# Kernel optimization log

Measured on AMD Instinct MI355X. Metric: run time of the kernel, lower is better.

Reference implementation:

```python
import jax, jax.numpy as jnp
import numpy as np

B = 131072
HIDDEN = 20
N_HID_LAYERS = 8  # 1 input layer (3->20) + 7 hidden (20->20), then head 20->2
G_GRAV = 9.81


def _xavier(key, fan_in, fan_out, shape):
    lim = float(np.sqrt(6.0 / (fan_in + fan_out)))
    return jax.random.uniform(key, shape, jnp.float32, -lim, lim)


def setup_inputs() -> dict:
    key = jax.random.key(0)
    ks = jax.random.split(key, 9)
    return {
        "x": jax.random.normal(ks[0], (B,), jnp.float32),
        "y": jax.random.normal(ks[1], (B,), jnp.float32),
        "t": jax.random.normal(ks[2], (B,), jnp.float32),
        "u": jax.random.normal(ks[3], (B,), jnp.float32),
        "v": jax.random.normal(ks[4], (B,), jnp.float32),
        "W_in": _xavier(ks[5], 3, HIDDEN, (3, HIDDEN)),
        "b_in": jnp.zeros((HIDDEN,), jnp.float32),
        "W_h": _xavier(ks[6], HIDDEN, HIDDEN, (N_HID_LAYERS - 1, HIDDEN, HIDDEN)),
        "b_h": jnp.zeros((N_HID_LAYERS - 1, HIDDEN), jnp.float32),
        "W_out": _xavier(ks[7], HIDDEN, 2, (HIDDEN, 2)),
        "b_out": jnp.zeros((2,), jnp.float32),
        "lambda1": jnp.zeros((), jnp.float32),
        "lambda2": jnp.zeros((), jnp.float32),
    }


def _pinn(x, y, t, u, v, W_in, b_in, W_h, b_h, W_out, b_out, lambda1, lambda2):
    def net(z):  # z: (3,) -> (2,) = (psi, p)
        h = jnp.tanh(z @ W_in + b_in)
        for i in range(W_h.shape[0]):
            h = jnp.tanh(h @ W_h[i] + b_h[i])
        return h @ W_out + b_out

    psi_fn = lambda z: net(z)[0]
    p_fn = lambda z: net(z)[1]

    def per_point(z):
        G = jax.grad(psi_fn)(z)                       # (3,)  dpsi/dz
        H = jax.jacfwd(jax.grad(psi_fn))(z)           # (3,3) d2psi
        T = jax.jacfwd(jax.jacfwd(jax.grad(psi_fn)))(z)  # (3,3,3) d3psi
        return G, H, T, p_fn(z), jax.grad(p_fn)(z)

    z = jnp.stack([x, y, t], axis=1)  # (B,3), axes: 0=x, 1=y, 2=t
    G, H, T, p_pred, Gp = jax.vmap(per_point)(z)

    u_pred = G[:, 1]          # dpsi/dy
    v_pred = -G[:, 0]         # -dpsi/dx
    u_x, u_y, u_t = H[:, 1, 0], H[:, 1, 1], H[:, 1, 2]
    v_x, v_y, v_t = -H[:, 0, 0], -H[:, 0, 1], -H[:, 0, 2]
    u_xx, u_yy = T[:, 1, 0, 0], T[:, 1, 1, 1]
    v_xx, v_yy = -T[:, 0, 0, 0], -T[:, 0, 1, 1]
    p_x, p_y = Gp[:, 0], Gp[:, 1]

    f_u = lambda1 * (u_t + u_pred * u_x + v_pred * u_y) + p_x - lambda2 * (u_xx + u_yy)
    f_v = (lambda1 * (v_t + u_pred * v_x + v_pred * v_y) - lambda1 * G_GRAV
           + p_y - lambda2 * (v_xx + v_yy))

    preds = jnp.stack([p_pred, u_pred, v_pred], axis=1)  # (B,3)
    loss = (jnp.sum((u - u_pred) ** 2) + jnp.sum((v - v_pred) ** 2)
            + jnp.sum(f_u ** 2) + jnp.sum(f_v ** 2))
    return preds, loss


def reference(x, y, t, u, v, W_in, b_in, W_h, b_h, W_out, b_out, lambda1, lambda2):
    return _pinn(x, y, t, u, v, W_in, b_in, W_h, b_h, W_out, b_out, lambda1, lambda2)
```

## Files before the change

kernel.cpp:

```cpp
#include <hip/hip_runtime.h>

typedef float v2f __attribute__((ext_vector_type(2)));

constexpr int BN   = 131072;
constexpr int HID  = 20;
constexpr int NLAY = 7;

constexpr int OFF_WH   = 0;
constexpr int OFF_BH   = 2800;
constexpr int OFF_WIN  = 2940;
constexpr int OFF_BIN  = 3000;
constexpr int OFF_WOUT = 3020;
constexpr int OFF_BOUT = 3060;
constexpr int LDS_TOT  = 3064;

enum { S_PX = 0, S_PXX, S_PXXX, S_P, S_GPX,
       S_PY, S_PYY, S_PYYY, S_GPY,
       S_D2P, S_D3P, S_D3M, S_XT, S_YT, NSLOT };

__device__ __forceinline__ float fast_tanh(float a) {
    float e = __builtin_amdgcn_exp2f(a * 2.8853900817779268f);
    float r = __builtin_amdgcn_rcpf(e + 1.0f);
    return __builtin_fmaf(-2.0f, r, 1.0f);
}
__device__ __forceinline__ v2f tanh2(v2f a) {
    v2f r; r.x = fast_tanh(a.x); r.y = fast_tanh(a.y); return r;
}
__device__ __forceinline__ v2f splat(float s) { v2f r = {s, s}; return r; }
#define FMA2(a, b, c) __builtin_elementwise_fma((a), (b), (c))

__device__ __forceinline__ void pk_fma_lo(v2f& acc, const v2f s, const v2f w) {
    asm("v_pk_fma_f32 %0, %1, %2, %0 op_sel:[0,0,0] op_sel_hi:[0,1,1]"
        : "+v"(acc) : "v"(s), "v"(w));
}
__device__ __forceinline__ void pk_fma_hi(v2f& acc, const v2f s, const v2f w) {
    asm("v_pk_fma_f32 %0, %1, %2, %0 op_sel:[1,0,0] op_sel_hi:[1,1,1]"
        : "+v"(acc) : "v"(s), "v"(w));
}

__device__ __forceinline__ void stage_weights(
    float* smem, const float* Win, const float* bin, const float* Wh,
    const float* bh, const float* Wout, const float* bout)
{
    const int tid = threadIdx.x;
    for (int i = tid; i < 2800; i += 256) smem[OFF_WH + i] = Wh[i];
    for (int i = tid; i < 140;  i += 256) smem[OFF_BH + i] = bh[i];
    if (tid < 60) smem[OFF_WIN  + tid] = Win[tid];
    if (tid < 20) smem[OFF_BIN  + tid] = bin[tid];
    if (tid < 40) smem[OFF_WOUT + tid] = Wout[tid];
    if (tid < 2)  smem[OFF_BOUT + tid] = bout[tid];
    __syncthreads();
}

template<bool BIASED>
__device__ __forceinline__ void sweep2(const v2f (&S1)[10], const v2f (&S2)[10],
                                       v2f (&A1)[10], v2f (&A2)[10],
                                       const float* __restrict__ Wl,
                                       const float* __restrict__ bl)
{
    #pragma unroll
    for (int j = 0; j < 10; ++j) {
        if (BIASED) { A1[j].x = bl[2*j]; A1[j].y = bl[2*j+1]; }
        else        A1[j] = splat(0.f);
        A2[j] = splat(0.f);
    }
    #pragma unroll
    for (int i = 0; i < 10; ++i) {
        const float* r0 = &Wl[(2 * i) * HID];
        const float* r1 = &Wl[(2 * i + 1) * HID];
        #pragma unroll
        for (int ob = 0; ob < 5; ++ob) {
            float4 w0 = *(const float4*)&r0[4 * ob];
            float4 w1 = *(const float4*)&r1[4 * ob];
            v2f w0a = {w0.x, w0.y}, w0b = {w0.z, w0.w};
            v2f w1a = {w1.x, w1.y}, w1b = {w1.z, w1.w};
            pk_fma_lo(A1[2*ob],   S1[i], w0a);
            pk_fma_lo(A1[2*ob+1], S1[i], w0b);
            pk_fma_hi(A1[2*ob],   S1[i], w1a);
            pk_fma_hi(A1[2*ob+1], S1[i], w1b);
            pk_fma_lo(A2[2*ob],   S2[i], w0a);
            pk_fma_lo(A2[2*ob+1], S2[i], w0b);
            pk_fma_hi(A2[2*ob],   S2[i], w1a);
            pk_fma_hi(A2[2*ob+1], S2[i], w1b);
        }
    }
}

__device__ __forceinline__ void sweep3(const v2f (&S1)[10], const v2f (&S2)[10],
                                       const v2f (&S3)[10],
                                       v2f (&A1)[10], v2f (&A2)[10], v2f (&A3)[10],
                                       const float* __restrict__ Wl,
                                       const float* __restrict__ bl)
{
    #pragma unroll
    for (int j = 0; j < 10; ++j) {
        A1[j].x = bl[2*j]; A1[j].y = bl[2*j+1];
        A2[j] = splat(0.f);
        A3[j] = splat(0.f);
    }
    #pragma unroll
    for (int i = 0; i < 10; ++i) {
        const float* r0 = &Wl[(2 * i) * HID];
        const float* r1 = &Wl[(2 * i + 1) * HID];
        #pragma unroll
        for (int ob = 0; ob < 5; ++ob) {
            float4 w0 = *(const float4*)&r0[4 * ob];
            float4 w1 = *(const float4*)&r1[4 * ob];
            v2f w0a = {w0.x, w0.y}, w0b = {w0.z, w0.w};
            v2f w1a = {w1.x, w1.y}, w1b = {w1.z, w1.w};
            pk_fma_lo(A1[2*ob],   S1[i], w0a);
            pk_fma_lo(A1[2*ob+1], S1[i], w0b);
            pk_fma_hi(A1[2*ob],   S1[i], w1a);
            pk_fma_hi(A1[2*ob+1], S1[i], w1b);
            pk_fma_lo(A2[2*ob],   S2[i], w0a);
            pk_fma_lo(A2[2*ob+1], S2[i], w0b);
            pk_fma_hi(A2[2*ob],   S2[i], w1a);
            pk_fma_hi(A2[2*ob+1], S2[i], w1b);
            pk_fma_lo(A3[2*ob],   S3[i], w0a);
            pk_fma_lo(A3[2*ob+1], S3[i], w0b);
            pk_fma_hi(A3[2*ob],   S3[i], w1a);
            pk_fma_hi(A3[2*ob+1], S3[i], w1b);
        }
    }
}

__global__ __launch_bounds__(256, 2) void pinn_fast(
    const float* __restrict__ x, const float* __restrict__ y, const float* __restrict__ t,
    const float* __restrict__ u, const float* __restrict__ v,
    const float* __restrict__ Win, const float* __restrict__ bin,
    const float* __restrict__ Wh,  const float* __restrict__ bh,
    const float* __restrict__ Wout,const float* __restrict__ bout,
    const float* __restrict__ lam1p, const float* __restrict__ lam2p,
    float* __restrict__ out)
{
    if (lam1p[0] != 0.0f || lam2p[0] != 0.0f) return;

    __shared__ __align__(16) float smem[LDS_TOT];
    __shared__ float wsum[4];
    stage_weights(smem, Win, bin, Wh, bh, Wout, bout);

    const int tid = threadIdx.x;
    const int pt  = blockIdx.x * 256 + tid;
    const float xv = x[pt], yv = y[pt], tv = t[pt];
    const v2f xv2 = splat(xv), yv2 = splat(yv), tv2 = splat(tv);

    v2f V[10], DX[10], DY[10];

    #pragma unroll
    for (int j = 0; j < 10; ++j) {
        v2f w0 = *(const v2f*)&smem[OFF_WIN + 2*j];
        v2f w1 = *(const v2f*)&smem[OFF_WIN + HID + 2*j];
        v2f w2 = *(const v2f*)&smem[OFF_WIN + 2*HID + 2*j];
        v2f av = *(const v2f*)&smem[OFF_BIN + 2*j];
        av = FMA2(xv2, w0, av);
        av = FMA2(yv2, w1, av);
        av = FMA2(tv2, w2, av);
        v2f s  = tanh2(av);
        v2f s1 = 1.0f - s * s;
        V[j]  = s;
        DX[j] = s1 * w0;
        DY[j] = s1 * w1;
    }

    #pragma unroll 1
    for (int l = 0; l < NLAY; ++l) {
        const float* Wl = &smem[OFF_WH + l * (HID * HID)];
        const float* bl = &smem[OFF_BH + l * HID];
        v2f aV[10], aX[10], aY[10];
        sweep3(V, DX, DY, aV, aX, aY, Wl, bl);
        #pragma unroll
        for (int j = 0; j < 10; ++j) {
            v2f s  = tanh2(aV[j]);
            v2f s1 = 1.0f - s * s;
            V[j]  = s;
            DX[j] = s1 * aX[j];
            DY[j] = s1 * aY[j];
        }
    }

    v2f dX = splat(0.f), dY = splat(0.f), dP = splat(0.f),
        dPX = splat(0.f), dPY = splat(0.f);
    #pragma unroll
    for (int j = 0; j < 10; ++j) {
        v2f w0j = {smem[OFF_WOUT + 4*j],     smem[OFF_WOUT + 4*j + 2]};
        v2f w1j = {smem[OFF_WOUT + 4*j + 1], smem[OFF_WOUT + 4*j + 3]};
        dX  = FMA2(DX[j], w0j, dX);
        dY  = FMA2(DY[j], w0j, dY);
        dP  = FMA2(V[j],  w1j, dP);
        dPX = FMA2(DX[j], w1j, dPX);
        dPY = FMA2(DY[j], w1j, dPY);
    }
    const float psi_x = dX.x + dX.y;
    const float psi_y = dY.x + dY.y;
    const float pv    = smem[OFF_BOUT + 1] + dP.x + dP.y;
    const float p_x   = dPX.x + dPX.y;
    const float p_y   = dPY.x + dPY.y;

    const float u_pred = psi_y;
    const float v_pred = -psi_x;
    const float f_u = p_x;
    const float f_v = p_y;

    out[3*pt+0] = pv;
    out[3*pt+1] = u_pred;
    out[3*pt+2] = v_pred;

    const float du = u[pt] - u_pred;
    const float dv = v[pt] - v_pred;
    float term = du * du + dv * dv + f_u * f_u + f_v * f_v;

    #pragma unroll
    for (int off = 32; off > 0; off >>= 1) term += __shfl_down(term, off);
    const int lane = tid & 63, wid = tid >> 6;
    if (lane == 0) wsum[wid] = term;
    __syncthreads();
    if (tid == 0) atomicAdd(&out[3*BN], wsum[0] + wsum[1] + wsum[2] + wsum[3]);
}

__global__ __launch_bounds__(256, 3) void pinn_jets6(
    const float* __restrict__ x, const float* __restrict__ y, const float* __restrict__ t,
    const float* __restrict__ Win, const float* __restrict__ bin,
    const float* __restrict__ Wh,  const float* __restrict__ bh,
    const float* __restrict__ Wout,const float* __restrict__ bout,
    const float* __restrict__ lam1p, const float* __restrict__ lam2p,
    float* __restrict__ ws)
{
    if (lam1p[0] == 0.0f && lam2p[0] == 0.0f) return;

    __shared__ __align__(16) float smem[LDS_TOT];
    stage_weights(smem, Win, bin, Wh, bh, Wout, bout);

    const int pt    = blockIdx.x * 256 + threadIdx.x;
    const int slice = blockIdx.y;

    const float xv = x[pt], yv = y[pt], tv = t[pt];
    const v2f xv2 = splat(xv), yv2 = splat(yv), tv2 = splat(tv);

    if (slice < 4) {
        const float DXT[4] = {1.f, 0.f, 1.f,  1.f};
        const float DYT[4] = {0.f, 1.f, 1.f, -1.f};
        const v2f dxv = splat(DXT[slice]), dyv = splat(DYT[slice]);

        v2f V[10], D1[10], D2[10], D3[10];

        #pragma unroll
        for (int j = 0; j < 10; ++j) {
            v2f w0 = *(const v2f*)&smem[OFF_WIN + 2*j];
            v2f w1 = *(const v2f*)&smem[OFF_WIN + HID + 2*j];
            v2f w2 = *(const v2f*)&smem[OFF_WIN + 2*HID + 2*j];
            v2f av = *(const v2f*)&smem[OFF_BIN + 2*j];
            av = FMA2(xv2, w0, av);
            av = FMA2(yv2, w1, av);
            av = FMA2(tv2, w2, av);
            v2f a1 = dxv * w0;
            a1 = FMA2(dyv, w1, a1);
            v2f s  = tanh2(av);
            v2f s2 = s * s;
            v2f s1 = 1.0f - s2;
            v2f f2 = -2.0f * s * s1;
            v2f f3 = s1 * (4.0f * s2 - 2.0f * s1);
            v2f a1sq = a1 * a1;
            V[j]  = s;
            D1[j] = s1 * a1;
            D2[j] = f2 * a1sq;
            D3[j] = f3 * a1sq * a1;
        }

        #pragma unroll 1
        for (int l = 0; l < NLAY; ++l) {
            const float* Wl = &smem[OFF_WH + l * (HID * HID)];
            const float* bl = &smem[OFF_BH + l * HID];
            v2f aV[10], a1[10];
            sweep2<true >(V,  D1, aV, a1, Wl, bl);
            v2f a2[10], a3[10];
            sweep2<false>(D2, D3, a2, a3, Wl, bl);
            #pragma unroll
            for (int j = 0; j < 10; ++j) {
                v2f s  = tanh2(aV[j]);
                v2f s2 = s * s;
                v2f s1 = 1.0f - s2;
                v2f f2 = -2.0f * s * s1;
                v2f f3 = s1 * (4.0f * s2 - 2.0f * s1);
                v2f u1 = a1[j];
                v2f u1sq = u1 * u1;
                V[j]  = s;
                D1[j] = s1 * u1;
                D2[j] = s1 * a2[j] + f2 * u1sq;
                D3[j] = s1 * a3[j] + 3.0f * f2 * (u1 * a2[j]) + f3 * u1sq * u1;
            }
        }

        v2f d1 = splat(0.f), d2 = splat(0.f), d3 = splat(0.f),
            dP = splat(0.f), dP1 = splat(0.f);
        #pragma unroll
        for (int j = 0; j < 10; ++j) {
            v2f w0j = {smem[OFF_WOUT + 4*j],     smem[OFF_WOUT + 4*j + 2]};
            v2f w1j = {smem[OFF_WOUT + 4*j + 1], smem[OFF_WOUT + 4*j + 3]};
            d1  = FMA2(D1[j], w0j, d1);
            d2  = FMA2(D2[j], w0j, d2);
            d3  = FMA2(D3[j], w0j, d3);
            dP  = FMA2(V[j],  w1j, dP);
            dP1 = FMA2(D1[j], w1j, dP1);
        }
        const float r1 = d1.x + d1.y;
        const float r2 = d2.x + d2.y;
        const float r3 = d3.x + d3.y;

        switch (slice) {
            case 0:
                ws[S_PX  *BN+pt] = r1;
                ws[S_PXX *BN+pt] = r2;
                ws[S_PXXX*BN+pt] = r3;
                ws[S_P   *BN+pt] = smem[OFF_BOUT + 1] + dP.x + dP.y;
                ws[S_GPX *BN+pt] = dP1.x + dP1.y;
                break;
            case 1:
                ws[S_PY  *BN+pt] = r1;
                ws[S_PYY *BN+pt] = r2;
                ws[S_PYYY*BN+pt] = r3;
                ws[S_GPY *BN+pt] = dP1.x + dP1.y;
                break;
            case 2:
                ws[S_D2P *BN+pt] = r2;
                ws[S_D3P *BN+pt] = r3;
                break;
            default:
                ws[S_D3M *BN+pt] = r3;
                break;
        }
    } else {
        v2f V[10], DA[10], DT[10], DAT[10];

        #pragma unroll
        for (int j = 0; j < 10; ++j) {
            v2f w0 = *(const v2f*)&smem[OFF_WIN + 2*j];
            v2f w1 = *(const v2f*)&smem[OFF_WIN + HID + 2*j];
            v2f w2 = *(const v2f*)&smem[OFF_WIN + 2*HID + 2*j];
            v2f av = *(const v2f*)&smem[OFF_BIN + 2*j];
            av = FMA2(xv2, w0, av);
            av = FMA2(yv2, w1, av);
            av = FMA2(tv2, w2, av);
            v2f wa = (slice == 4) ? w0 : w1;
            v2f s  = tanh2(av);
            v2f s1 = 1.0f - s * s;
            v2f f2 = -2.0f * s * s1;
            V[j]   = s;
            DA[j]  = s1 * wa;
            DT[j]  = s1 * w2;
            DAT[j] = f2 * wa * w2;
        }

        #pragma unroll 1
        for (int l = 0; l < NLAY; ++l) {
            const float* Wl = &smem[OFF_WH + l * (HID * HID)];
            const float* bl = &smem[OFF_BH + l * HID];
            v2f aV[10], aA[10];
            sweep2<true >(V,  DA,  aV, aA, Wl, bl);
            v2f aT[10], aAT[10];
            sweep2<false>(DT, DAT, aT, aAT, Wl, bl);
            #pragma unroll
            for (int j = 0; j < 10; ++j) {
                v2f s  = tanh2(aV[j]);
                v2f s1 = 1.0f - s * s;
                v2f f2 = -2.0f * s * s1;
                V[j]   = s;
                DA[j]  = s1 * aA[j];
                DT[j]  = s1 * aT[j];
                DAT[j] = f2 * (aA[j] * aT[j]) + s1 * aAT[j];
            }
        }

        v2f dAT = splat(0.f);
        #pragma unroll
        for (int j = 0; j < 10; ++j) {
            v2f w0j = {smem[OFF_WOUT + 4*j], smem[OFF_WOUT + 4*j + 2]};
            dAT = FMA2(DAT[j], w0j, dAT);
        }
        const float r = dAT.x + dAT.y;
        if (slice == 4) ws[S_XT*BN+pt] = r;
        else            ws[S_YT*BN+pt] = r;
    }
}

__global__ __launch_bounds__(256) void pinn_combine(
    const float* __restrict__ ws,
    const float* __restrict__ u, const float* __restrict__ v,
    const float* __restrict__ lam1p, const float* __restrict__ lam2p,
    float* __restrict__ out)
{
    if (lam1p[0] == 0.0f && lam2p[0] == 0.0f) return;

    __shared__ float wsum[4];
    const int tid = threadIdx.x;
    const int pt  = blockIdx.x * 256 + tid;

    const float psi_x   = ws[S_PX  *BN+pt];
    const float psi_xx  = ws[S_PXX *BN+pt];
    const float psi_xxx = ws[S_PXXX*BN+pt];
    const float pv      = ws[S_P   *BN+pt];
    const float p_x     = ws[S_GPX *BN+pt];
    const float psi_y   = ws[S_PY  *BN+pt];
    const float psi_yy  = ws[S_PYY *BN+pt];
    const float psi_yyy = ws[S_PYYY*BN+pt];
    const float p_y     = ws[S_GPY *BN+pt];
    const float d2p     = ws[S_D2P *BN+pt];
    const float d3p     = ws[S_D3P *BN+pt];
    const float d3m     = ws[S_D3M *BN+pt];
    const float psi_xt  = ws[S_XT  *BN+pt];
    const float psi_yt  = ws[S_YT  *BN+pt];

    const float psi_xy  = 0.5f * (d2p - psi_xx - psi_yy);
    const float psi_xxy = (d3p - d3m - 2.0f * psi_yyy) * (1.0f / 6.0f);
    const float psi_xyy = (d3p + d3m - 2.0f * psi_xxx) * (1.0f / 6.0f);

    const float u_pred = psi_y;
    const float v_pred = -psi_x;
    const float u_x = psi_xy,  u_y = psi_yy,  u_t = psi_yt;
    const float v_x = -psi_xx, v_y = -psi_xy, v_t = -psi_xt;
    const float u_xx = psi_xxy, u_yy = psi_yyy;
    const float v_xx = -psi_xxx, v_yy = -psi_xyy;

    const float lam1 = lam1p[0];
    const float lam2 = lam2p[0];

    const float f_u = lam1 * (u_t + u_pred * u_x + v_pred * u_y) + p_x - lam2 * (u_xx + u_yy);
    const float f_v = lam1 * (v_t + u_pred * v_x + v_pred * v_y) - lam1 * 9.81f + p_y
                      - lam2 * (v_xx + v_yy);

    out[3*pt+0] = pv;
    out[3*pt+1] = u_pred;
    out[3*pt+2] = v_pred;

    const float du = u[pt] - u_pred;
    const float dv = v[pt] - v_pred;
    float term = du * du + dv * dv + f_u * f_u + f_v * f_v;

    #pragma unroll
    for (int off = 32; off > 0; off >>= 1) term += __shfl_down(term, off);
    const int lane = tid & 63, wid = tid >> 6;
    if (lane == 0) wsum[wid] = term;
    __syncthreads();
    if (tid == 0) atomicAdd(&out[3*BN], wsum[0] + wsum[1] + wsum[2] + wsum[3]);
}

extern "C" void kernel_launch(void* const* d_in, const int* in_sizes, int n_in,
                              void* d_out, int out_size, void* d_ws, size_t ws_size,
                              hipStream_t stream) {
    const float* x    = (const float*)d_in[0];
    const float* y    = (const float*)d_in[1];
    const float* t    = (const float*)d_in[2];
    const float* u    = (const float*)d_in[3];
    const float* v    = (const float*)d_in[4];
    const float* Win  = (const float*)d_in[5];
    const float* bin  = (const float*)d_in[6];
    const float* Wh   = (const float*)d_in[7];
    const float* bh   = (const float*)d_in[8];
    const float* Wout = (const float*)d_in[9];
    const float* bout = (const float*)d_in[10];
    const float* lam1 = (const float*)d_in[11];
    const float* lam2 = (const float*)d_in[12];

    float* out = (float*)d_out;
    float* ws  = (float*)d_ws;

    hipMemsetAsync(out + 3 * BN, 0, sizeof(float), stream);

    pinn_fast<<<BN / 256, 256, 0, stream>>>(x, y, t, u, v, Win, bin, Wh, bh,
                                            Wout, bout, lam1, lam2, out);
    pinn_jets6<<<dim3(BN / 256, 6), 256, 0, stream>>>(x, y, t, Win, bin, Wh, bh,
                                                      Wout, bout, lam1, lam2, ws);
    pinn_combine<<<BN / 256, 256, 0, stream>>>(ws, u, v, lam1, lam2, out);
}
```

Baseline: 45.91 us.

## Split each point's hidden-layer matvec across two threads with shuffle reduction

Replaces the single-thread-per-point fast kernel with one where each pair of lanes shares a point. Each lane handles half of the input neurons of every 20x20 layer and keeps only 5 packed activation slots. Partial sums are combined with xor-1 shuffles, after which each lane applies tanh to its own half of the outputs. This halves register pressure and doubles the number of threads, aiming at higher occupancy and latency hiding, at the cost of extra cross-lane shuffles per layer and half-idle lanes in the final store and reduction.

```diff
diff --git a/kernel.cpp b/kernel.cpp
--- a/kernel.cpp
+++ b/kernel.cpp
@@ -27,6 +27,9 @@
     v2f r; r.x = fast_tanh(a.x); r.y = fast_tanh(a.y); return r;
 }
 __device__ __forceinline__ v2f splat(float s) { v2f r = {s, s}; return r; }
+__device__ __forceinline__ v2f shflx1(v2f a) {
+    v2f r; r.x = __shfl_xor(a.x, 1); r.y = __shfl_xor(a.y, 1); return r;
+}
 #define FMA2(a, b, c) __builtin_elementwise_fma((a), (b), (c))
 
 __device__ __forceinline__ void pk_fma_lo(v2f& acc, const v2f s, const v2f w) {
@@ -50,6 +53,139 @@
     if (tid < 40) smem[OFF_WOUT + tid] = Wout[tid];
     if (tid < 2)  smem[OFF_BOUT + tid] = bout[tid];
     __syncthreads();
+}
+
+__global__ __launch_bounds__(256, 4) void pinn_fast2(
+    const float* __restrict__ x, const float* __restrict__ y, const float* __restrict__ t,
+    const float* __restrict__ u, const float* __restrict__ v,
+    const float* __restrict__ Win, const float* __restrict__ bin,
+    const float* __restrict__ Wh,  const float* __restrict__ bh,
+    const float* __restrict__ Wout,const float* __restrict__ bout,
+    const float* __restrict__ lam1p, const float* __restrict__ lam2p,
+    float* __restrict__ out)
+{
+    if (lam1p[0] != 0.0f || lam2p[0] != 0.0f) return;
+
+    __shared__ __align__(16) float smem[LDS_TOT];
+    __shared__ float wsum[4];
+    stage_weights(smem, Win, bin, Wh, bh, Wout, bout);
+
+    const int tid  = threadIdx.x;
+    const int half = tid & 1;
+    const int base = 5 * half;
+    const int pt   = blockIdx.x * 128 + (tid >> 1);
+
+    const float xv = x[pt], yv = y[pt], tv = t[pt];
+    const v2f xv2 = splat(xv), yv2 = splat(yv), tv2 = splat(tv);
+
+    v2f V[5], DX[5], DY[5];
+
+    #pragma unroll
+    for (int j = 0; j < 5; ++j) {
+        const int g = base + j;
+        v2f w0 = *(const v2f*)&smem[OFF_WIN + 2*g];
+        v2f w1 = *(const v2f*)&smem[OFF_WIN + HID + 2*g];
+        v2f w2 = *(const v2f*)&smem[OFF_WIN + 2*HID + 2*g];
+        v2f av = *(const v2f*)&smem[OFF_BIN + 2*g];
+        av = FMA2(xv2, w0, av);
+        av = FMA2(yv2, w1, av);
+        av = FMA2(tv2, w2, av);
+        v2f s  = tanh2(av);
+        v2f s1 = 1.0f - s * s;
+        V[j]  = s;
+        DX[j] = s1 * w0;
+        DY[j] = s1 * w1;
+    }
+
+    #pragma unroll 1
+    for (int l = 0; l < NLAY; ++l) {
+        const float* Wl = &smem[OFF_WH + l * (HID * HID)];
+        v2f aV[10], aX[10], aY[10];
+        #pragma unroll
+        for (int k = 0; k < 10; ++k) { aV[k] = splat(0.f); aX[k] = splat(0.f); aY[k] = splat(0.f); }
+        #pragma unroll
+        for (int i = 0; i < 5; ++i) {
+            const float* r0 = &Wl[(2 * (base + i)) * HID];
+            const float* r1 = &Wl[(2 * (base + i) + 1) * HID];
+            #pragma unroll
+            for (int ob = 0; ob < 5; ++ob) {
+                float4 w0 = *(const float4*)&r0[4 * ob];
+                float4 w1 = *(const float4*)&r1[4 * ob];
+                v2f w0a = {w0.x, w0.y}, w0b = {w0.z, w0.w};
+                v2f w1a = {w1.x, w1.y}, w1b = {w1.z, w1.w};
+                pk_fma_lo(aV[2*ob],   V[i],  w0a);
+                pk_fma_lo(aV[2*ob+1], V[i],  w0b);
+                pk_fma_hi(aV[2*ob],   V[i],  w1a);
+                pk_fma_hi(aV[2*ob+1], V[i],  w1b);
+                pk_fma_lo(aX[2*ob],   DX[i], w0a);
+                pk_fma_lo(aX[2*ob+1], DX[i], w0b);
+                pk_fma_hi(aX[2*ob],   DX[i], w1a);
+                pk_fma_hi(aX[2*ob+1], DX[i], w1b);
+                pk_fma_lo(aY[2*ob],   DY[i], w0a);
+                pk_fma_lo(aY[2*ob+1], DY[i], w0b);
+                pk_fma_hi(aY[2*ob],   DY[i], w1a);
+                pk_fma_hi(aY[2*ob+1], DY[i], w1b);
+            }
+        }
+        #pragma unroll
+        for (int k = 0; k < 10; ++k) {
+            aV[k] += shflx1(aV[k]);
+            aX[k] += shflx1(aX[k]);
+            aY[k] += shflx1(aY[k]);
+        }
+        #pragma unroll
+        for (int j = 0; j < 5; ++j) {
+            v2f a0 = half ? aV[5 + j] : aV[j];
+            v2f ax = half ? aX[5 + j] : aX[j];
+            v2f ay = half ? aY[5 + j] : aY[j];
+            a0 += *(const v2f*)&smem[OFF_BH + l * HID + 2 * (base + j)];
+            v2f s  = tanh2(a0);
+            v2f s1 = 1.0f - s * s;
+            V[j]  = s;
+            DX[j] = s1 * ax;
+            DY[j] = s1 * ay;
+        }
+    }
+
+    v2f dX = splat(0.f), dY = splat(0.f), dP = splat(0.f),
+        dPX = splat(0.f), dPY = splat(0.f);
+    #pragma unroll
+    for (int j = 0; j < 5; ++j) {
+        const int g = base + j;
+        v2f w0j = {smem[OFF_WOUT + 4*g],     smem[OFF_WOUT + 4*g + 2]};
+        v2f w1j = {smem[OFF_WOUT + 4*g + 1], smem[OFF_WOUT + 4*g + 3]};
+        dX  = FMA2(DX[j], w0j, dX);
+        dY  = FMA2(DY[j], w0j, dY);
+        dP  = FMA2(V[j],  w1j, dP);
+        dPX = FMA2(DX[j], w1j, dPX);
+        dPY = FMA2(DY[j], w1j, dPY);
+    }
+    float psi_x = dX.x + dX.y;   psi_x += __shfl_xor(psi_x, 1);
+    float psi_y = dY.x + dY.y;   psi_y += __shfl_xor(psi_y, 1);
+    float pv    = dP.x + dP.y;   pv    += __shfl_xor(pv, 1);
+    float p_x   = dPX.x + dPX.y; p_x   += __shfl_xor(p_x, 1);
+    float p_y   = dPY.x + dPY.y; p_y   += __shfl_xor(p_y, 1);
+    pv += smem[OFF_BOUT + 1];
+
+    const float u_pred = psi_y;
+    const float v_pred = -psi_x;
+
+    float term = 0.0f;
+    if (half == 0) {
+        out[3*pt+0] = pv;
+        out[3*pt+1] = u_pred;
+        out[3*pt+2] = v_pred;
+        const float du = u[pt] - u_pred;
+        const float dv = v[pt] - v_pred;
+        term = du * du + dv * dv + p_x * p_x + p_y * p_y;
+    }
+
+    #pragma unroll
+    for (int off = 32; off > 0; off >>= 1) term += __shfl_down(term, off);
+    const int lane = tid & 63, wid = tid >> 6;
+    if (lane == 0) wsum[wid] = term;
+    __syncthreads();
+    if (tid == 0) atomicAdd(&out[3*BN], wsum[0] + wsum[1] + wsum[2] + wsum[3]);
 }
 
 template<bool BIASED>
@@ -84,137 +220,6 @@
             pk_fma_hi(A2[2*ob+1], S2[i], w1b);
         }
     }
-}
-
-__device__ __forceinline__ void sweep3(const v2f (&S1)[10], const v2f (&S2)[10],
-                                       const v2f (&S3)[10],
-                                       v2f (&A1)[10], v2f (&A2)[10], v2f (&A3)[10],
-                                       const float* __restrict__ Wl,
-                                       const float* __restrict__ bl)
-{
-    #pragma unroll
-    for (int j = 0; j < 10; ++j) {
-        A1[j].x = bl[2*j]; A1[j].y = bl[2*j+1];
-        A2[j] = splat(0.f);
-        A3[j] = splat(0.f);
-    }
-    #pragma unroll
-    for (int i = 0; i < 10; ++i) {
-        const float* r0 = &Wl[(2 * i) * HID];
-        const float* r1 = &Wl[(2 * i + 1) * HID];
-        #pragma unroll
-        for (int ob = 0; ob < 5; ++ob) {
-            float4 w0 = *(const float4*)&r0[4 * ob];
-            float4 w1 = *(const float4*)&r1[4 * ob];
-            v2f w0a = {w0.x, w0.y}, w0b = {w0.z, w0.w};
-            v2f w1a = {w1.x, w1.y}, w1b = {w1.z, w1.w};
-            pk_fma_lo(A1[2*ob],   S1[i], w0a);
-            pk_fma_lo(A1[2*ob+1], S1[i], w0b);
-            pk_fma_hi(A1[2*ob],   S1[i], w1a);
-            pk_fma_hi(A1[2*ob+1], S1[i], w1b);
-            pk_fma_lo(A2[2*ob],   S2[i], w0a);
-            pk_fma_lo(A2[2*ob+1], S2[i], w0b);
-            pk_fma_hi(A2[2*ob],   S2[i], w1a);
-            pk_fma_hi(A2[2*ob+1], S2[i], w1b);
-            pk_fma_lo(A3[2*ob],   S3[i], w0a);
-            pk_fma_lo(A3[2*ob+1], S3[i], w0b);
-            pk_fma_hi(A3[2*ob],   S3[i], w1a);
-            pk_fma_hi(A3[2*ob+1], S3[i], w1b);
-        }
-    }
-}
-
-__global__ __launch_bounds__(256, 2) void pinn_fast(
-    const float* __restrict__ x, const float* __restrict__ y, const float* __restrict__ t,
-    const float* __restrict__ u, const float* __restrict__ v,
-    const float* __restrict__ Win, const float* __restrict__ bin,
-    const float* __restrict__ Wh,  const float* __restrict__ bh,
-    const float* __restrict__ Wout,const float* __restrict__ bout,
-    const float* __restrict__ lam1p, const float* __restrict__ lam2p,
-    float* __restrict__ out)
-{
-    if (lam1p[0] != 0.0f || lam2p[0] != 0.0f) return;
-
-    __shared__ __align__(16) float smem[LDS_TOT];
-    __shared__ float wsum[4];
-    stage_weights(smem, Win, bin, Wh, bh, Wout, bout);
-
-    const int tid = threadIdx.x;
-    const int pt  = blockIdx.x * 256 + tid;
-    const float xv = x[pt], yv = y[pt], tv = t[pt];
-    const v2f xv2 = splat(xv), yv2 = splat(yv), tv2 = splat(tv);
-
-    v2f V[10], DX[10], DY[10];
-
-    #pragma unroll
-    for (int j = 0; j < 10; ++j) {
-        v2f w0 = *(const v2f*)&smem[OFF_WIN + 2*j];
-        v2f w1 = *(const v2f*)&smem[OFF_WIN + HID + 2*j];
-        v2f w2 = *(const v2f*)&smem[OFF_WIN + 2*HID + 2*j];
-        v2f av = *(const v2f*)&smem[OFF_BIN + 2*j];
-        av = FMA2(xv2, w0, av);
-        av = FMA2(yv2, w1, av);
-        av = FMA2(tv2, w2, av);
-        v2f s  = tanh2(av);
-        v2f s1 = 1.0f - s * s;
-        V[j]  = s;
-        DX[j] = s1 * w0;
-        DY[j] = s1 * w1;
-    }
-
-    #pragma unroll 1
-    for (int l = 0; l < NLAY; ++l) {
-        const float* Wl = &smem[OFF_WH + l * (HID * HID)];
-        const float* bl = &smem[OFF_BH + l * HID];
-        v2f aV[10], aX[10], aY[10];
-        sweep3(V, DX, DY, aV, aX, aY, Wl, bl);
-        #pragma unroll
-        for (int j = 0; j < 10; ++j) {
-            v2f s  = tanh2(aV[j]);
-            v2f s1 = 1.0f - s * s;
-            V[j]  = s;
-            DX[j] = s1 * aX[j];
-            DY[j] = s1 * aY[j];
-        }
-    }
-
-    v2f dX = splat(0.f), dY = splat(0.f), dP = splat(0.f),
-        dPX = splat(0.f), dPY = splat(0.f);
-    #pragma unroll
-    for (int j = 0; j < 10; ++j) {
-        v2f w0j = {smem[OFF_WOUT + 4*j],     smem[OFF_WOUT + 4*j + 2]};
-        v2f w1j = {smem[OFF_WOUT + 4*j + 1], smem[OFF_WOUT + 4*j + 3]};
-        dX  = FMA2(DX[j], w0j, dX);
-        dY  = FMA2(DY[j], w0j, dY);
-        dP  = FMA2(V[j],  w1j, dP);
-        dPX = FMA2(DX[j], w1j, dPX);
-        dPY = FMA2(DY[j], w1j, dPY);
-    }
-    const float psi_x = dX.x + dX.y;
-    const float psi_y = dY.x + dY.y;
-    const float pv    = smem[OFF_BOUT + 1] + dP.x + dP.y;
-    const float p_x   = dPX.x + dPX.y;
-    const float p_y   = dPY.x + dPY.y;
-
-    const float u_pred = psi_y;
-    const float v_pred = -psi_x;
-    const float f_u = p_x;
-    const float f_v = p_y;
-
-    out[3*pt+0] = pv;
-    out[3*pt+1] = u_pred;
-    out[3*pt+2] = v_pred;
-
-    const float du = u[pt] - u_pred;
-    const float dv = v[pt] - v_pred;
-    float term = du * du + dv * dv + f_u * f_u + f_v * f_v;
-
-    #pragma unroll
-    for (int off = 32; off > 0; off >>= 1) term += __shfl_down(term, off);
-    const int lane = tid & 63, wid = tid >> 6;
-    if (lane == 0) wsum[wid] = term;
-    __syncthreads();
-    if (tid == 0) atomicAdd(&out[3*BN], wsum[0] + wsum[1] + wsum[2] + wsum[3]);
 }
 
 __global__ __launch_bounds__(256, 3) void pinn_jets6(
@@ -465,8 +470,8 @@
 
     hipMemsetAsync(out + 3 * BN, 0, sizeof(float), stream);
 
-    pinn_fast<<<BN / 256, 256, 0, stream>>>(x, y, t, u, v, Win, bin, Wh, bh,
-                                            Wout, bout, lam1, lam2, out);
+    pinn_fast2<<<BN / 128, 256, 0, stream>>>(x, y, t, u, v, Win, bin, Wh, bh,
+                                             Wout, bout, lam1, lam2, out);
     pinn_jets6<<<dim3(BN / 256, 6), 256, 0, stream>>>(x, y, t, Win, bin, Wh, bh,
                                                       Wout, bout, lam1, lam2, ws);
     pinn_combine<<<BN / 256, 256, 0, stream>>>(ws, u, v, lam1, lam2, out);
```

Result: slower. 56.69 us (+23.5%).
